# Kernel tuning notes

Hardware: AMD Instinct MI355X
Metric: run time of the kernel (lower is better)

Reference implementation:

```python
import jax, jax.numpy as jnp
import numpy as np

B, L, C, H, T = 4096, 32, 28, 512, 32


def setup_inputs() -> dict:
    key = jax.random.key(0)
    ks = jax.random.split(key, 10)
    s = 0.1
    return dict(
        input=jax.random.normal(ks[0], (B, L, C), jnp.float32),
        unpacked_masks=jnp.ones((B, L, 1), jnp.float32),
        bias_mat=jax.random.normal(ks[1], (B, L), jnp.float32),
        conv1_w=jax.random.normal(ks[2], (C, C, 3), jnp.float32) * s,  # OIH
        conv1_b=jnp.zeros((C,), jnp.float32),
        conv_w=jax.random.normal(ks[3], (1, C, 1), jnp.float32) * s,
        conv_b=jnp.zeros((1,), jnp.float32),
        w_ih=jax.random.normal(ks[4], (4 * H, C), jnp.float32) * s,
        w_hh=jax.random.normal(ks[5], (4 * H, H), jnp.float32) * s,
        b_ih=jnp.zeros((4 * H,), jnp.float32),
        b_hh=jnp.concatenate([jnp.zeros(H), jnp.ones(H), jnp.zeros(2 * H)]).astype(jnp.float32),  # forget-gate bias = 1 as in weights_init
        fc1_w=jax.random.normal(ks[6], (1, H), jnp.float32) * s,
        fc1_b=jnp.zeros((1,), jnp.float32),
        conv2_w=jax.random.normal(ks[7], (1, H, 1), jnp.float32) * s,
        conv2_b=jnp.zeros((1,), jnp.float32),
    )


def reference(input, unpacked_masks, bias_mat, conv1_w, conv1_b, conv_w, conv_b,
              w_ih, w_hh, b_ih, b_hh, fc1_w, fc1_b, conv2_w, conv2_b):
    b, l, c = input.shape
    # residual conv block: conv1d(28->28,k3,pad1) -> mask -> elu -> +input
    x_ncl = jnp.transpose(input, (0, 2, 1))
    y = jax.lax.conv_general_dilated(x_ncl, conv1_w, (1,), 'SAME',
                                     dimension_numbers=('NCH', 'OIH', 'NCH'))
    y = jnp.transpose(y + conv1_b[None, :, None], (0, 2, 1))
    x = jax.nn.elu(y * unpacked_masks) + input  # [B,L,C]
    # u_a: 1x1 conv (28->1) == per-position linear, then mask -> [B,L,1]
    u_a = (jnp.einsum('blc,c->bl', x, conv_w[0, :, 0]) + conv_b)[..., None] * unpacked_masks
    bias = bias_mat.reshape(b, l, 1)

    def step(carry, _):
        h, cstate = carry
        w_a = (h @ fc1_w.T + fc1_b)[:, :, None]                 # [B,1,1]
        attn = jax.nn.leaky_relu(u_a + w_a) + bias              # [B,L,1]
        attn = jax.nn.softmax(attn, axis=1)                     # softmax over sequence
        context = jnp.einsum('bl,blc->bc', attn[..., 0], x)     # [B,C]
        gates = context @ w_ih.T + b_ih + h @ w_hh.T + b_hh     # [B,4H]
        i, f, g, o = jnp.split(gates, 4, axis=1)                # torch LSTMCell gate order
        cstate = jax.nn.sigmoid(f) * cstate + jax.nn.sigmoid(i) * jnp.tanh(g)
        h = jax.nn.sigmoid(o) * jnp.tanh(cstate)
        return (h, cstate), h

    h0 = jnp.zeros((b, w_hh.shape[1]), input.dtype)
    (_, _), hs = jax.lax.scan(step, (h0, h0), None, length=T)   # [T,B,H]
    all_hidden = jnp.transpose(hs, (1, 0, 2))                   # [B,T,H]
    # dropout layers are identity in eval; conv2 is 1x1 conv (512->1)
    out = (jnp.einsum('bth,h->bt', all_hidden, conv2_w[0, :, 0]) + conv2_b)[..., None]
    return out * unpacked_masks
```

## Files before the change

kernel.cpp:

```cpp
#include <hip/hip_runtime.h>
#include <hip/hip_bf16.h>

#define B_N 4096
#define L_N 32
#define C_N 28
#define H_N 512
#define T_N 32
#define G_N 2048
#define CHA 34
#define CHSH 4096
#define ABLK (CHA * CHSH)
#define XS 29

typedef __attribute__((ext_vector_type(2))) float f32x2;
typedef __attribute__((ext_vector_type(4))) float f32x4;
typedef __attribute__((ext_vector_type(8))) short s16x8;

static constexpr size_t OFF_WF = 0;
static constexpr size_t AB_ONE = (size_t)32 * ABLK * 2;
static constexpr size_t OFF_AB = OFF_WF + (size_t)16 * ABLK * 2;
static constexpr size_t OFF_X  = OFF_AB + 2 * AB_ONE;
static constexpr size_t OFF_UA = OFF_X + (size_t)B_N * L_N * C_N * 4;
static constexpr size_t OFF_BS = OFF_UA + (size_t)B_N * L_N * 4;
static constexpr size_t OFF_AC = OFF_BS + 8192;
static constexpr size_t ACC_HALF = (size_t)32 * B_N * 4;
static constexpr size_t OFF_CS = OFF_AC + 2 * ACC_HALF;
static constexpr size_t WS_NEED = OFF_CS + (size_t)B_N * H_N * 4;

__device__ __forceinline__ short bfbits(__hip_bfloat16 b) {
    union { __hip_bfloat16 b; short s; } v; v.b = b; return v.s;
}
__device__ __forceinline__ float sigmoidf_(float x) { return 1.f / (1.f + __expf(-x)); }
__device__ __forceinline__ float tanhf_(float x) {
    float ax = fabsf(x), e = __expf(-2.f * ax);
    float t = (1.f - e) / (1.f + e);
    return x < 0.f ? -t : t;
}

__global__ __launch_bounds__(256) void fill_out(float* out, float v) {
    int i = blockIdx.x * 256 + threadIdx.x;
    if (i < B_N * 32) out[i] = v;
}

__global__ __launch_bounds__(256) void prep_x(const float* __restrict__ input,
                       const float* __restrict__ mask,
                       const float* __restrict__ w1, const float* __restrict__ b1,
                       const float* __restrict__ cw, const float* __restrict__ cb,
                       float* __restrict__ x, float* __restrict__ ua)
{
    __shared__ float sin[8 * L_N * XS];
    __shared__ float sxb[8 * L_N * XS];
    const float* src = input + (size_t)blockIdx.x * (8 * L_N * C_N);
    for (int i = threadIdx.x; i < 8 * L_N * C_N; i += 256) {
        int lr = i / (L_N * C_N);
        int rem = i - lr * (L_N * C_N);
        int l = rem / C_N, c = rem - l * C_N;
        sin[lr * (L_N * XS) + l * XS + c] = src[i];
    }
    __syncthreads();

    int idx = blockIdx.x * 256 + threadIdx.x;
    int l = idx & 31;
    int wv = threadIdx.x >> 5;
    const float* inb = sin + wv * (L_N * XS);
    float m = mask[idx];

    float x0r[C_N], xm1[C_N], xp1[C_N];
    #pragma unroll
    for (int i = 0; i < C_N; ++i) x0r[i] = inb[l * XS + i];
    #pragma unroll
    for (int i = 0; i < C_N; ++i) {
        float up = __shfl_up(x0r[i], 1, 32);
        float dn = __shfl_down(x0r[i], 1, 32);
        xm1[i] = (l > 0)  ? up : 0.f;
        xp1[i] = (l < 31) ? dn : 0.f;
    }

    float uacc = 0.f;
    float* sxrow = sxb + wv * (L_N * XS) + l * XS;
    #pragma unroll 2
    for (int o = 0; o < C_N; ++o) {
        const float* wo = w1 + o * (C_N * 3);
        float y0 = b1[o], y1 = 0.f, y2 = 0.f;
        #pragma unroll
        for (int i = 0; i < C_N; ++i) {
            y0 += wo[i * 3 + 0] * xm1[i];
            y1 += wo[i * 3 + 1] * x0r[i];
            y2 += wo[i * 3 + 2] * xp1[i];
        }
        float y = (y0 + y1 + y2) * m;
        float e = (y > 0.f) ? y : (__expf(y) - 1.f);
        float xv = e + inb[l * XS + o];
        sxrow[o] = xv;
        uacc += xv * cw[o];
    }
    ua[idx] = (uacc + cb[0]) * m;
    __syncthreads();
    float* xdst = x + (size_t)blockIdx.x * (8 * L_N * C_N);
    for (int i = threadIdx.x; i < 8 * L_N * C_N; i += 256) {
        int lr = i / (L_N * C_N);
        int rem = i - lr * (L_N * C_N);
        int l2 = rem / C_N, c = rem - l2 * C_N;
        xdst[i] = sxb[lr * (L_N * XS) + l2 * XS + c];
    }
}

__global__ __launch_bounds__(256) void prep_wf(const float* __restrict__ w_ih,
                                               const float* __restrict__ w_hh,
                                               short* __restrict__ Wf)
{
    int blk = blockIdx.x;
    int n128 = blk / CHA, c = blk % CHA;
    bool lo = (c >= 17);
    int kbase = (lo ? (c - 17) : c) * 32;
    short* dst = Wf + ((size_t)n128 * CHA + c) * CHSH;
    for (int g = threadIdx.x; g < 512; g += 256) {
        int j = g >> 6, lane = g & 63;
        int gate = j & 3;
        int unit = n128 * 32 + (j >> 2) * 16 + (lane & 15);
        int srow = gate * H_N + unit;
        int kg = lane >> 4;
        s16x8 out;
        #pragma unroll
        for (int b2 = 0; b2 < 8; ++b2) {
            int k = kbase + kg * 8 + b2;
            float v = 0.f;
            if (k < 512) v = w_hh[(size_t)srow * H_N + k];
            else if (k < 540) v = w_ih[srow * C_N + (k - 512)];
            __hip_bfloat16 hi = __float2bfloat16(v);
            if (lo) out[b2] = bfbits(__float2bfloat16(v - __bfloat162float(hi)));
            else    out[b2] = bfbits(hi);
        }
        *(s16x8*)(dst + g * 8) = out;
    }
}

__global__ void prep_bs(const float* __restrict__ b_ih, const float* __restrict__ b_hh,
                        float* __restrict__ bsum)
{
    int p = blockIdx.x * 256 + threadIdx.x;
    if (p < G_N) {
        int unit = p >> 2, gate = p & 3;
        bsum[p] = b_ih[gate * H_N + unit] + b_hh[gate * H_N + unit];
    }
}

__global__ void prep_zero(unsigned int* __restrict__ a32, float* __restrict__ cst,
                          float* __restrict__ acc)
{
    int idx = blockIdx.x * blockDim.x + threadIdx.x;
    if (idx < B_N * 1088) a32[idx] = 0u;
    if (idx < B_N * H_N) cst[idx] = 0.f;
    if (idx < 2 * 32 * B_N) acc[idx] = 0.f;
}

struct RParams {
    const float* mask;
    const float* bias_mat;
    const float* fc1_w;
    const float* fc1_b;
    const float* conv2_w;
    const float* conv2_b;
    const short* Wf;
    const short* Ain;
    short* Aout;
    const float* x;
    const float* ua;
    const float* bsum;
    float* accW;
    float* accO;
    float* cstate;
    float* out;
};

__global__ __launch_bounds__(256) void ctx_step(RParams P, int t)
{
    __shared__ float sx[4][L_N * C_N];

    const int lane = threadIdx.x & 63;
    const int wave = threadIdx.x >> 6;
    const int row  = blockIdx.x * 4 + wave;

    f32x2 st[7];
    const float* xrow = P.x + (size_t)row * (L_N * C_N);
    #pragma unroll
    for (int q = 0; q < 7; ++q) st[q] = *(const f32x2*)(xrow + (q * 64 + lane) * 2);

    float v = (lane < 32) ? P.accW[row * 32 + lane] : P.accO[row * 32 + (lane - 32)];
    #pragma unroll
    for (int off = 1; off <= 16; off <<= 1) v += __shfl_xor(v, off);
    float aW = __shfl(v, 0);
    float aO = __shfl(v, 32);

    if (t > 0 && lane == 0)
        P.out[row * T_N + (t - 1)] = (aO + P.conv2_b[0]) * P.mask[row * L_N + (t - 1)];

    if (t < T_N) {
        float w_a = aW + P.fc1_b[0];
        int l32 = lane & 31;
        float e = P.ua[row * L_N + l32] + w_a;
        e = (e > 0.f) ? e : 0.01f * e;
        e += P.bias_mat[row * L_N + l32];
        float mx = e;
        #pragma unroll
        for (int off = 16; off > 0; off >>= 1) mx = fmaxf(mx, __shfl_xor(mx, off, 32));
        float pexp = __expf(e - mx);
        float ssum = pexp;
        #pragma unroll
        for (int off = 16; off > 0; off >>= 1) ssum += __shfl_xor(ssum, off, 32);
        float p = pexp / ssum;

        #pragma unroll
        for (int q = 0; q < 7; ++q)
            *(f32x2*)(&sx[wave][(q * 64 + lane) * 2]) = st[q];

        int cc = (lane < C_N) ? lane : 0;
        float ctx = 0.f;
        #pragma unroll
        for (int l = 0; l < L_N; ++l) {
            float al = __shfl(p, l);
            ctx += al * sx[wave][l * C_N + cc];
        }
        if (lane < C_N) {
            int m128 = row >> 7, mt = (row & 127) >> 4, r = row & 15;
            int flane = r + 16 * (lane >> 3);
            short* base = P.Aout + (size_t)m128 * ABLK + mt * 512 + flane * 8 + (lane & 7);
            __hip_bfloat16 hi = __float2bfloat16(ctx);
            base[16 * CHSH] = bfbits(hi);
            base[33 * CHSH] = bfbits(__float2bfloat16(ctx - __bfloat162float(hi)));
        }
    }
}

#define STG_BUF 24576

__global__ __launch_bounds__(256, 3) void gemm_cell_step(RParams P)
{
    __shared__ __align__(16) char smem[49152];

    const int tid  = threadIdx.x;
    const int lane = tid & 63;
    const int wave = tid >> 6;
    const int bid  = blockIdx.x;
    const int m64 = bid & 63, n = bid >> 6;
    const int m128 = m64 >> 1, half = m64 & 1;
    const int wm = wave >> 1, wn = wave & 1;

    const short* Af = P.Ain + (size_t)m128 * ABLK + half * 2048;
    const short* Wg = P.Wf  + (size_t)n * ABLK;

    char* bufp0 = smem;
    char* bufp1 = smem + STG_BUF;

    auto stage = [&](char* lbuf, int kk) {
        if (wave == 0) {
            const short* gh = Af + (size_t)kk * CHSH + lane * 8;
            const short* gl = Af + (size_t)(17 + kk) * CHSH + lane * 8;
            #pragma unroll
            for (int r = 0; r < 4; ++r)
                __builtin_amdgcn_global_load_lds(
                    (const __attribute__((address_space(1))) void*)(gh + r * 512),
                    (__attribute__((address_space(3))) void*)(lbuf + r * 1024), 16, 0, 0);
            #pragma unroll
            for (int r = 0; r < 4; ++r)
                __builtin_amdgcn_global_load_lds(
                    (const __attribute__((address_space(1))) void*)(gl + r * 512),
                    (__attribute__((address_space(3))) void*)(lbuf + 4096 + r * 1024), 16, 0, 0);
        } else if (wave == 1) {
            const short* gp = Wg + (size_t)kk * CHSH + lane * 8;
            #pragma unroll
            for (int r = 0; r < 8; ++r)
                __builtin_amdgcn_global_load_lds(
                    (const __attribute__((address_space(1))) void*)(gp + r * 512),
                    (__attribute__((address_space(3))) void*)(lbuf + 8192 + r * 1024), 16, 0, 0);
        } else if (wave == 2) {
            const short* gp = Wg + (size_t)(17 + kk) * CHSH + lane * 8;
            #pragma unroll
            for (int r = 0; r < 8; ++r)
                __builtin_amdgcn_global_load_lds(
                    (const __attribute__((address_space(1))) void*)(gp + r * 512),
                    (__attribute__((address_space(3))) void*)(lbuf + 16384 + r * 1024), 16, 0, 0);
        }
    };

    int aoff[2], woff[4];
    #pragma unroll
    for (int i = 0; i < 2; ++i) aoff[i] = ((wm * 2 + i) * 64 + lane) * 16;
    #pragma unroll
    for (int j = 0; j < 4; ++j) woff[j] = ((wn * 4 + j) * 64 + lane) * 16;

    f32x4 acc[2][4];
    #pragma unroll
    for (int i = 0; i < 2; ++i)
        #pragma unroll
        for (int j = 0; j < 4; ++j)
            acc[i][j] = (f32x4){0.f, 0.f, 0.f, 0.f};

    s16x8 RA[12], RB[12];
    auto ldfr = [&](const char* b, s16x8 (&R)[12]) {
        #pragma unroll
        for (int i = 0; i < 2; ++i) {
            R[i]     = *(const s16x8*)(b + aoff[i]);
            R[2 + i] = *(const s16x8*)(b + 4096 + aoff[i]);
        }
        #pragma unroll
        for (int j = 0; j < 4; ++j) {
            R[4 + j] = *(const s16x8*)(b + 8192 + woff[j]);
            R[8 + j] = *(const s16x8*)(b + 16384 + woff[j]);
        }
    };
    auto domm = [&](s16x8 (&R)[12]) {
        #pragma unroll
        for (int i = 0; i < 2; ++i)
            #pragma unroll
            for (int j = 0; j < 4; ++j)
                acc[i][j] = __builtin_amdgcn_mfma_f32_16x16x32_bf16(R[i], R[4 + j], acc[i][j], 0, 0, 0);
        #pragma unroll
        for (int i = 0; i < 2; ++i)
            #pragma unroll
            for (int j = 0; j < 4; ++j)
                acc[i][j] = __builtin_amdgcn_mfma_f32_16x16x32_bf16(R[2 + i], R[4 + j], acc[i][j], 0, 0, 0);
        #pragma unroll
        for (int i = 0; i < 2; ++i)
            #pragma unroll
            for (int j = 0; j < 4; ++j)
                acc[i][j] = __builtin_amdgcn_mfma_f32_16x16x32_bf16(R[i], R[8 + j], acc[i][j], 0, 0, 0);
    };
    auto step = [&](int kk, s16x8 (&Rc)[12], s16x8 (&Rn)[12], char* bcur, char* bnext) {
        asm volatile("s_waitcnt vmcnt(0) lgkmcnt(0)" ::: "memory");
        __builtin_amdgcn_s_barrier();
        __builtin_amdgcn_sched_barrier(0);
        if (kk + 2 <= 16) stage(bcur, kk + 2);
        if (kk + 1 <= 16) ldfr(bnext, Rn);
        __builtin_amdgcn_sched_barrier(0);
        __builtin_amdgcn_s_setprio(1);
        domm(Rc);
        __builtin_amdgcn_s_setprio(0);
        __builtin_amdgcn_sched_barrier(0);
    };

    stage(bufp0, 0);
    asm volatile("s_waitcnt vmcnt(0)" ::: "memory");
    __builtin_amdgcn_s_barrier();
    stage(bufp1, 1);
    ldfr(bufp0, RA);

    for (int kp = 0; kp < 8; ++kp) {
        step(2 * kp,     RA, RB, bufp0, bufp1);
        step(2 * kp + 1, RB, RA, bufp1, bufp0);
    }
    step(16, RA, RB, bufp0, bufp1);

    __syncthreads();
    short* hasm = (short*)smem;
    {
        int u15 = lane & 15, rq = lane >> 4;
        int unit = n * 32 + wn * 16 + u15;
        float cpre[2][4];
        #pragma unroll
        for (int i = 0; i < 2; ++i)
            #pragma unroll
            for (int r = 0; r < 4; ++r)
                cpre[i][r] = P.cstate[(size_t)(m64 * 64 + wm * 32 + i * 16 + rq * 4 + r) * H_N + unit];
        f32x4 bsv = *(const f32x4*)(P.bsum + unit * 4);
        float f1v = P.fc1_w[unit];
        float c2v = P.conv2_w[unit];
        const int fl16 = 16 * (wn * 2 + (u15 >> 3));
        const int slot = u15 & 7;
        #pragma unroll
        for (int i = 0; i < 2; ++i) {
            #pragma unroll
            for (int r = 0; r < 4; ++r) {
                int grow = m64 * 64 + wm * 32 + i * 16 + rq * 4 + r;
                float pi = acc[i][0][r] + bsv.x;
                float pf = acc[i][1][r] + bsv.y;
                float pg = acc[i][2][r] + bsv.z;
                float po = acc[i][3][r] + bsv.w;
                float c = sigmoidf_(pf) * cpre[i][r] + sigmoidf_(pi) * tanhf_(pg);
                P.cstate[(size_t)grow * H_N + unit] = c;
                float h = sigmoidf_(po) * tanhf_(c);
                __hip_bfloat16 hi = __float2bfloat16(h);
                int fo = (wm * 2 + i) * 512 + (rq * 4 + r + fl16) * 8 + slot;
                hasm[fo]        = bfbits(hi);
                hasm[2048 + fo] = bfbits(__float2bfloat16(h - __bfloat162float(hi)));
                float wd = f1v * h, od = c2v * h;
                #pragma unroll
                for (int off = 8; off > 0; off >>= 1) {
                    wd += __shfl_xor(wd, off);
                    od += __shfl_xor(od, off);
                }
                if (u15 == 0) {
                    P.accW[(size_t)grow * 32 + (n * 2 + wn)] = wd;
                    P.accO[(size_t)grow * 32 + (n * 2 + wn)] = od;
                }
            }
        }
    }
    __syncthreads();
    short* dhi = P.Aout + (size_t)m128 * ABLK + (size_t)n * CHSH + half * 2048;
    short* dlo = P.Aout + (size_t)m128 * ABLK + (size_t)(17 + n) * CHSH + half * 2048;
    *(s16x8*)(dhi + tid * 8) = *(const s16x8*)(hasm + tid * 8);
    *(s16x8*)(dlo + tid * 8) = *(const s16x8*)(hasm + 2048 + tid * 8);
}

extern "C" void kernel_launch(void* const* d_in, const int* in_sizes, int n_in,
                              void* d_out, int out_size, void* d_ws, size_t ws_size,
                              hipStream_t stream)
{
    float* out = (float*)d_out;
    if (ws_size < WS_NEED) { fill_out<<<512, 256, 0, stream>>>(out, 4000.f); return; }

    const float* input = (const float*)d_in[0];
    const float* mask  = (const float*)d_in[1];
    const float* biasm = (const float*)d_in[2];
    const float* w1    = (const float*)d_in[3];
    const float* b1    = (const float*)d_in[4];
    const float* cw    = (const float*)d_in[5];
    const float* cb    = (const float*)d_in[6];
    const float* w_ih  = (const float*)d_in[7];
    const float* w_hh  = (const float*)d_in[8];
    const float* b_ih  = (const float*)d_in[9];
    const float* b_hh  = (const float*)d_in[10];
    const float* fc1w  = (const float*)d_in[11];
    const float* fc1b  = (const float*)d_in[12];
    const float* c2w   = (const float*)d_in[13];
    const float* c2b   = (const float*)d_in[14];

    char* ws = (char*)d_ws;
    short* Wf = (short*)(ws + OFF_WF);
    short* A0 = (short*)(ws + OFF_AB);
    short* A1 = (short*)(ws + OFF_AB + AB_ONE);
    float* x    = (float*)(ws + OFF_X);
    float* ua   = (float*)(ws + OFF_UA);
    float* bsum = (float*)(ws + OFF_BS);
    float* accW = (float*)(ws + OFF_AC);
    float* accO = (float*)(ws + OFF_AC + ACC_HALF);
    float* cst  = (float*)(ws + OFF_CS);

    prep_x<<<(B_N * L_N) / 256, 256, 0, stream>>>(input, mask, w1, b1, cw, cb, x, ua);
    prep_wf<<<16 * CHA, 256, 0, stream>>>(w_ih, w_hh, Wf);
    prep_bs<<<(G_N + 255) / 256, 256, 0, stream>>>(b_ih, b_hh, bsum);
    prep_zero<<<(B_N * 1088 + 255) / 256, 256, 0, stream>>>((unsigned int*)A0, cst, accW);

    RParams P;
    P.mask = mask; P.bias_mat = biasm; P.fc1_w = fc1w; P.fc1_b = fc1b;
    P.conv2_w = c2w; P.conv2_b = c2b; P.Wf = Wf;
    P.x = x; P.ua = ua; P.bsum = bsum; P.accW = accW; P.accO = accO;
    P.cstate = cst; P.out = out;

    short* bufs[2] = { A0, A1 };
    for (int t = 0; t < T_N; ++t) {
        P.Ain  = bufs[t & 1];
        P.Aout = bufs[t & 1];
        ctx_step<<<B_N / 4, 256, 0, stream>>>(P, t);
        P.Ain  = bufs[t & 1];
        P.Aout = bufs[(t + 1) & 1];
        gemm_cell_step<<<1024, 256, 0, stream>>>(P);
    }
    P.Ain = bufs[T_N & 1];
    P.Aout = bufs[T_N & 1];
    ctx_step<<<B_N / 4, 256, 0, stream>>>(P, T_N);
}
```

Baseline: 1.418 ms.

## Switch GEMM step to triple-buffered LDS pipeline with partial vmcnt waits

```diff
diff --git a/kernel.cpp b/kernel.cpp
--- a/kernel.cpp
+++ b/kernel.cpp
@@ -234,9 +234,9 @@
 
 #define STG_BUF 24576
 
-__global__ __launch_bounds__(256, 3) void gemm_cell_step(RParams P)
-{
-    __shared__ __align__(16) char smem[49152];
+__global__ __launch_bounds__(256, 2) void gemm_cell_step(RParams P)
+{
+    __shared__ __align__(16) char smem[73728];
 
     const int tid  = threadIdx.x;
     const int lane = tid & 63;
@@ -249,8 +249,9 @@
     const short* Af = P.Ain + (size_t)m128 * ABLK + half * 2048;
     const short* Wg = P.Wf  + (size_t)n * ABLK;
 
-    char* bufp0 = smem;
-    char* bufp1 = smem + STG_BUF;
+    char* b0 = smem;
+    char* b1 = smem + STG_BUF;
+    char* b2 = smem + 2 * STG_BUF;
 
     auto stage = [&](char* lbuf, int kk) {
         if (wave == 0) {
@@ -296,20 +297,24 @@
         for (int j = 0; j < 4; ++j)
             acc[i][j] = (f32x4){0.f, 0.f, 0.f, 0.f};
 
-    s16x8 RA[12], RB[12];
-    auto ldfr = [&](const char* b, s16x8 (&R)[12]) {
+    auto step = [&](int kk, char* bread, char* bstage, bool last) {
+        if (!last) asm volatile("s_waitcnt vmcnt(8)" ::: "memory");
+        else       asm volatile("s_waitcnt vmcnt(0)" ::: "memory");
+        __builtin_amdgcn_s_barrier();
+        __builtin_amdgcn_sched_barrier(0);
+        if (kk + 2 <= 16) stage(bstage, kk + 2);
+        s16x8 R[12];
         #pragma unroll
         for (int i = 0; i < 2; ++i) {
-            R[i]     = *(const s16x8*)(b + aoff[i]);
-            R[2 + i] = *(const s16x8*)(b + 4096 + aoff[i]);
+            R[i]     = *(const s16x8*)(bread + aoff[i]);
+            R[2 + i] = *(const s16x8*)(bread + 4096 + aoff[i]);
         }
         #pragma unroll
         for (int j = 0; j < 4; ++j) {
-            R[4 + j] = *(const s16x8*)(b + 8192 + woff[j]);
-            R[8 + j] = *(const s16x8*)(b + 16384 + woff[j]);
-        }
-    };
-    auto domm = [&](s16x8 (&R)[12]) {
+            R[4 + j] = *(const s16x8*)(bread + 8192 + woff[j]);
+            R[8 + j] = *(const s16x8*)(bread + 16384 + woff[j]);
+        }
+        __builtin_amdgcn_s_setprio(1);
         #pragma unroll
         for (int i = 0; i < 2; ++i)
             #pragma unroll
@@ -325,31 +330,21 @@
             #pragma unroll
             for (int j = 0; j < 4; ++j)
                 acc[i][j] = __builtin_amdgcn_mfma_f32_16x16x32_bf16(R[i], R[8 + j], acc[i][j], 0, 0, 0);
-    };
-    auto step = [&](int kk, s16x8 (&Rc)[12], s16x8 (&Rn)[12], char* bcur, char* bnext) {
-        asm volatile("s_waitcnt vmcnt(0) lgkmcnt(0)" ::: "memory");
-        __builtin_amdgcn_s_barrier();
-        __builtin_amdgcn_sched_barrier(0);
-        if (kk + 2 <= 16) stage(bcur, kk + 2);
-        if (kk + 1 <= 16) ldfr(bnext, Rn);
-        __builtin_amdgcn_sched_barrier(0);
-        __builtin_amdgcn_s_setprio(1);
-        domm(Rc);
         __builtin_amdgcn_s_setprio(0);
         __builtin_amdgcn_sched_barrier(0);
     };
 
-    stage(bufp0, 0);
-    asm volatile("s_waitcnt vmcnt(0)" ::: "memory");
-    __builtin_amdgcn_s_barrier();
-    stage(bufp1, 1);
-    ldfr(bufp0, RA);
-
-    for (int kp = 0; kp < 8; ++kp) {
-        step(2 * kp,     RA, RB, bufp0, bufp1);
-        step(2 * kp + 1, RB, RA, bufp1, bufp0);
-    }
-    step(16, RA, RB, bufp0, bufp1);
+    stage(b0, 0);
+    stage(b1, 1);
+
+    #pragma unroll
+    for (int kp = 0; kp < 5; ++kp) {
+        step(3 * kp + 0, b0, b2, false);
+        step(3 * kp + 1, b1, b0, false);
+        step(3 * kp + 2, b2, b1, false);
+    }
+    step(15, b0, b2, false);
+    step(16, b1, b0, true);
 
     __syncthreads();
     short* hasm = (short*)smem;
```

New measurement: 1.478 ms. +4.2%, slower.
